# Performance work log

Hardware: AMD Instinct MI355X
Metric: run time of the kernel (lower is better)

## Reference

```python
import jax, jax.numpy as jnp
import numpy as np

NUM_HEADS = 8
ALPHA = 4.0  # spikingjelly sigmoid surrogate default

@jax.custom_vjp
def spike(x):
    return (x >= 0.0).astype(x.dtype)

def _spike_fwd(x):
    return spike(x), x

def _spike_bwd(x, g):
    s = jax.nn.sigmoid(ALPHA * x)
    return (g * ALPHA * s * (1.0 - s),)

spike.defvjp(_spike_fwd, _spike_bwd)

def lif(x, v_th=1.0, tau=2.0):
    # multi-step LIF over leading T dim; v_reset=0, hard reset, detach_reset
    def step(v, xt):
        h = v + (xt - v) / tau
        s = spike(h - v_th)
        v_new = h * (1.0 - jax.lax.stop_gradient(s))
        return v_new, s
    _, out = jax.lax.scan(step, jnp.zeros_like(x[0]), x)
    return out

def bn(x, gamma, beta, mean, var, eps=1e-5):
    # inference BatchNorm2d on (N,C,H,W)
    inv = gamma / jnp.sqrt(var + eps)
    return x * inv[None, :, None, None] + (beta - mean * inv)[None, :, None, None]

def conv1x1(x, w, b=None):
    # x: (N,C,H,W), w: (O,C)
    y = jnp.einsum('nchw,oc->nohw', x, w)
    if b is not None:
        y = y + b[None, :, None, None]
    return y

def setup_inputs() -> dict:
    key = jax.random.key(0)
    ks = jax.random.split(key, 20)
    T, B, C, H, W = 4, 32, 384, 14, 14
    d = {
        'x': jax.random.normal(ks[0], (T, B, C, H, W), jnp.float32),
        'q_w': jax.random.normal(ks[1], (C, C), jnp.float32) * (1.0 / np.sqrt(C)),
        'q_gamma': jax.random.uniform(ks[2], (C,), jnp.float32),
        'q_beta': jax.random.normal(ks[3], (C,), jnp.float32) * 0.1,
        'q_mean': jax.random.normal(ks[4], (C,), jnp.float32) * 0.1,
        'q_var': jax.random.uniform(ks[5], (C,), jnp.float32) + 0.5,
        'k_w': jax.random.normal(ks[6], (C, C), jnp.float32) * (1.0 / np.sqrt(C)),
        'k_gamma': jax.random.uniform(ks[7], (C,), jnp.float32),
        'k_beta': jax.random.normal(ks[8], (C,), jnp.float32) * 0.1,
        'k_mean': jax.random.normal(ks[9], (C,), jnp.float32) * 0.1,
        'k_var': jax.random.uniform(ks[10], (C,), jnp.float32) + 0.5,
        'proj_w': jax.random.normal(ks[11], (C, C), jnp.float32) * (1.0 / np.sqrt(C)),
        'proj_b': jax.random.normal(ks[12], (C,), jnp.float32) * 0.1,
        'proj_gamma': jax.random.uniform(ks[13], (C,), jnp.float32),
        'proj_beta': jax.random.normal(ks[14], (C,), jnp.float32) * 0.1,
        'proj_mean': jax.random.normal(ks[15], (C,), jnp.float32) * 0.1,
        'proj_var': jax.random.uniform(ks[16], (C,), jnp.float32) + 0.5,
    }
    return d

def reference(x, q_w, q_gamma, q_beta, q_mean, q_var,
              k_w, k_gamma, k_beta, k_mean, k_var,
              proj_w, proj_b, proj_gamma, proj_beta, proj_mean, proj_var):
    T, B, C, H, W = x.shape
    dh = C // NUM_HEADS
    xf = x.reshape(T * B, C, H, W)
    # Q branch: conv1x1 -> BN -> multistep LIF
    q = bn(conv1x1(xf, q_w), q_gamma, q_beta, q_mean, q_var).reshape(T, B, C, H, W)
    q = lif(q).reshape(T, B, NUM_HEADS, dh, H, W)
    # K branch
    k = bn(conv1x1(xf, k_w), k_gamma, k_beta, k_mean, k_var).reshape(T, B, C, H, W)
    k = lif(k).reshape(T, B, NUM_HEADS, dh, H, W)
    # sum-pool attention: sum q over head feature dim, spike it, gate k
    qs = jnp.sum(q, axis=3, keepdims=True)          # (T,B,heads,1,H,W)
    attn = lif(qs, v_th=0.5)
    y = (attn * k).reshape(T * B, C, H, W)
    # output projection: conv1x1(+bias) -> BN -> LIF
    y = bn(conv1x1(y, proj_w, proj_b), proj_gamma, proj_beta, proj_mean, proj_var)
    y = lif(y.reshape(T, B, C, H, W))
    return y
```

## Files before the change

### kernel.cpp

```cpp
#include <hip/hip_runtime.h>

#define C_DIM 384
#define S_DIM 196
#define CS_   (C_DIM * S_DIM)
#define BCS   (32 * CS_)
#define NELEM (128 * CS_)
#define NBS   6272

typedef _Float16 half8  __attribute__((ext_vector_type(8)));
typedef float    floatx4 __attribute__((ext_vector_type(4)));

__device__ __forceinline__ void gl_lds16(const _Float16* g, _Float16* l) {
    __builtin_amdgcn_global_load_lds(
        (const __attribute__((address_space(1))) unsigned int*)g,
        (__attribute__((address_space(3))) unsigned int*)l, 16, 0, 0);
}

__global__ __launch_bounds__(256)
void split_w(const float* __restrict__ qw, const float* __restrict__ kw,
             const float* __restrict__ pw,
             const float* qg, const float* qb, const float* qm, const float* qv,
             const float* kg, const float* kb, const float* km, const float* kv,
             _Float16* __restrict__ Wq0, _Float16* __restrict__ Wq1,
             _Float16* __restrict__ Wp0, _Float16* __restrict__ Wp1,
             float2* __restrict__ invsh)
{
    const int i = blockIdx.x * 256 + threadIdx.x;
    const int NQ = 768 * C_DIM;
    if (i < NQ) {
        const int o = i / C_DIM, c = i - o * C_DIM;
        const float v = (o < 384) ? qw[o * C_DIM + c] : kw[(o - 384) * C_DIM + c];
        const _Float16 h0 = (_Float16)v;
        Wq0[i] = h0;
        Wq1[i] = (_Float16)((v - (float)h0) * 4096.0f);
    } else if (i < NQ + C_DIM * C_DIM) {
        const int j = i - NQ;
        const float v = pw[j];
        const _Float16 h0 = (_Float16)v;
        Wp0[j] = h0;
        Wp1[j] = (_Float16)((v - (float)h0) * 4096.0f);
    }
    if (i < 768) {
        float g, b, m, vv;
        if (i < 384) { g = qg[i]; b = qb[i]; m = qm[i]; vv = qv[i]; }
        else         { g = kg[i-384]; b = kb[i-384]; m = km[i-384]; vv = kv[i-384]; }
        const float inv = g / sqrtf(vv + 1e-5f);
        invsh[i] = make_float2(inv, b - m * inv);
    }
}

__global__ __launch_bounds__(256)
void split_x(const float* __restrict__ X,
             _Float16* __restrict__ X0, _Float16* __restrict__ X1)
{
    __shared__ float tile[32][201];
    const int tb = blockIdx.x;
    const int tt = tb >> 5, b = tb & 31;
    const int c0 = blockIdx.y * 32;
    const int t  = threadIdx.x;
    for (int idx = t; idx < 32 * S_DIM; idx += 256) {
        const int cc = idx / S_DIM, s = idx - cc * S_DIM;
        tile[cc][s] = X[(size_t)tb * CS_ + (c0 + cc) * S_DIM + s];
    }
    __syncthreads();
    for (int idx = t; idx < 32 * S_DIM; idx += 256) {
        const int s = idx >> 5, cc = idx & 31;
        const float v = tile[cc][s];
        const _Float16 h0 = (_Float16)v;
        const size_t off = ((size_t)(b * S_DIM + s) * 4 + tt) * C_DIM + c0 + cc;
        X0[off] = h0;
        X1[off] = (_Float16)((v - (float)h0) * 4096.0f);
    }
}

__global__ __launch_bounds__(256, 3)
void qk_mfma(const _Float16* __restrict__ A0, const _Float16* __restrict__ A1,
             const _Float16* __restrict__ B0, const _Float16* __restrict__ B1,
             const float2* __restrict__ invsh,
             unsigned char* __restrict__ spkQ, unsigned char* __restrict__ spkK)
{
    __shared__ __align__(16) _Float16 As0[128 * 32];
    __shared__ __align__(16) _Float16 As1[128 * 32];
    __shared__ __align__(16) _Float16 Bs0[128 * 32];
    __shared__ __align__(16) _Float16 Bs1[128 * 32];

    const int t    = threadIdx.x;
    const int wave = t >> 6, lane = t & 63;
    const int m0 = blockIdx.x * 128;
    const int o0 = blockIdx.y * 128;

    const int wR   = wave * 32;
    const int sRow = lane >> 2;
    const int sCol = (((lane & 3) ^ ((sRow >> 1) & 3))) << 3;

    const int lo = lane & 15, quad = lane >> 4;
    const int oq = (wave >> 1) * 64, mq = (wave & 1) * 64;
    const int rdC = (quad ^ ((lo >> 1) & 3)) << 3;

    floatx4 acc[4][4];
    #pragma unroll
    for (int i = 0; i < 4; ++i)
        #pragma unroll
        for (int j = 0; j < 4; ++j) acc[i][j] = (floatx4)0.0f;

    for (int kt = 0; kt < 12; ++kt) {
        __syncthreads();
        const int kb = kt * 32;
        #pragma unroll
        for (int u = 0; u < 2; ++u) {
            const int R = wR + u * 16;
            const size_t ga = (size_t)(o0 + R + sRow) * C_DIM + kb + sCol;
            const size_t gb = (size_t)(m0 + R + sRow) * C_DIM + kb + sCol;
            gl_lds16(A0 + ga, &As0[R * 32]);
            gl_lds16(A1 + ga, &As1[R * 32]);
            gl_lds16(B0 + gb, &Bs0[R * 32]);
            gl_lds16(B1 + gb, &Bs1[R * 32]);
        }
        __syncthreads();

        half8 a0F[4], a1F[4], b0F[4], b1F[4];
        #pragma unroll
        for (int i = 0; i < 4; ++i) {
            const int ra = (oq + i * 16 + lo) * 32 + rdC;
            a0F[i] = *(const half8*)&As0[ra];
            a1F[i] = *(const half8*)&As1[ra];
        }
        #pragma unroll
        for (int j = 0; j < 4; ++j) {
            const int rb = (mq + j * 16 + lo) * 32 + rdC;
            b0F[j] = *(const half8*)&Bs0[rb];
            b1F[j] = *(const half8*)&Bs1[rb];
        }
        #pragma unroll
        for (int i = 0; i < 4; ++i) {
            const half8 aS = a0F[i] * (_Float16)4096.0f;
            #pragma unroll
            for (int j = 0; j < 4; ++j) {
                acc[i][j] = __builtin_amdgcn_mfma_f32_16x16x32_f16(
                    a0F[i], b1F[j], acc[i][j], 0, 0, 0);
                acc[i][j] = __builtin_amdgcn_mfma_f32_16x16x32_f16(
                    a1F[i], b0F[j], acc[i][j], 0, 0, 0);
                acc[i][j] = __builtin_amdgcn_mfma_f32_16x16x32_f16(
                    aS,     b0F[j], acc[i][j], 0, 0, 0);
            }
        }
    }

    __syncthreads();
    unsigned char* sb = (unsigned char*)As0;
    #pragma unroll
    for (int i = 0; i < 4; ++i) {
        #pragma unroll
        for (int r = 0; r < 4; ++r) {
            const int o = o0 + oq + i * 16 + quad * 4 + r;
            const float2 is = invsh[o];
            const float inv = is.x * (1.0f / 4096.0f);
            const float sh  = is.y;
            #pragma unroll
            for (int j = 0; j < 4; ++j) {
                const float xv = acc[i][j][r] * inv + sh;
                const int g = lane & ~3;
                const float x0 = __shfl(xv, g + 0);
                const float x1 = __shfl(xv, g + 1);
                const float x2 = __shfl(xv, g + 2);
                const float x3 = __shfl(xv, g + 3);
                if ((lane & 3) == 0) {
                    float xs[4] = {x0, x1, x2, x3};
                    float v = 0.0f; int bits = 0;
                    #pragma unroll
                    for (int tt = 0; tt < 4; ++tt) {
                        const float h = v + (xs[tt] - v) * 0.5f;
                        const int sp = (h >= 1.0f);
                        v = sp ? 0.0f : h;
                        bits |= sp << tt;
                    }
                    const int bsl = (mq + j * 16 + lo) >> 2;
                    const int ol  = oq + i * 16 + quad * 4 + r;
                    sb[bsl * 128 + ol] = (unsigned char)bits;
                }
            }
        }
    }
    __syncthreads();
    {
        unsigned char* base = (o0 < 384) ? spkQ : spkK;
        const int o0c = (o0 < 384) ? o0 : o0 - 384;
        const int row = t >> 3, ch = t & 7;
        const uint4 v = *(const uint4*)&sb[row * 128 + ch * 16];
        *(uint4*)(base + (size_t)((m0 >> 2) + row) * C_DIM + o0c + ch * 16) = v;
    }
}

__global__ __launch_bounds__(256)
void attn_compute(const unsigned char* __restrict__ spkQ,
                  unsigned char* __restrict__ attnB)
{
    const int idx = blockIdx.x * 256 + threadIdx.x;
    if (idx >= NBS * 8) return;
    const int bs = idx >> 3, head = idx & 7;
    const unsigned long long* p =
        (const unsigned long long*)(spkQ + (size_t)bs * C_DIM + head * 48);
    int qs[4] = {0, 0, 0, 0};
    #pragma unroll
    for (int u = 0; u < 6; ++u) {
        const unsigned long long v = p[u];
        qs[0] += __popcll(v & 0x0101010101010101ull);
        qs[1] += __popcll(v & 0x0202020202020202ull);
        qs[2] += __popcll(v & 0x0404040404040404ull);
        qs[3] += __popcll(v & 0x0808080808080808ull);
    }
    float va = 0.0f;
    int bits = 0;
    #pragma unroll
    for (int t = 0; t < 4; ++t) {
        const float h = va + ((float)qs[t] - va) * 0.5f;
        const int a = (h >= 0.5f);
        va = a ? 0.0f : h;
        bits |= a << t;
    }
    attnB[idx] = (unsigned char)bits;
}

__global__ __launch_bounds__(256, 3)
void proj_mfma(const _Float16* __restrict__ A0, const _Float16* __restrict__ A1,
               const unsigned char* __restrict__ spkK,
               const unsigned char* __restrict__ attnB,
               const float* __restrict__ bias, const float2* __restrict__ invsh,
               float* __restrict__ out)
{
    __shared__ __align__(16) _Float16 As0[128 * 32];
    __shared__ __align__(16) _Float16 As1[128 * 32];
    __shared__ __align__(16) _Float16 Bs0[128 * 32];

    const int t    = threadIdx.x;
    const int wave = t >> 6, lane = t & 63;
    const int m0 = blockIdx.x * 128;
    const int o0 = blockIdx.y * 128;

    const int wR   = wave * 32;
    const int sRow = lane >> 2;
    const int sCol = (((lane & 3) ^ ((sRow >> 1) & 3))) << 3;
    const int gC8  = (lane & 3) << 3;
    const int pC8  = sCol;

    const int lo = lane & 15, quad = lane >> 4;
    const int oq = (wave >> 1) * 64, mq = (wave & 1) * 64;
    const int rdC = (quad ^ ((lo >> 1) & 3)) << 3;

    const int bsL[2] = { (m0 + wR +  0 + sRow) >> 2, (m0 + wR + 16 + sRow) >> 2 };
    const int ttL    = (m0 + wR + sRow) & 3;

    floatx4 acc[4][4];
    #pragma unroll
    for (int i = 0; i < 4; ++i)
        #pragma unroll
        for (int j = 0; j < 4; ++j) acc[i][j] = (floatx4)0.0f;

    unsigned long long rk[2];
    int rab[2];
    {
        const int head0 = gC8 / 48;
        #pragma unroll
        for (int u = 0; u < 2; ++u) {
            rk[u]  = *(const unsigned long long*)(spkK + (size_t)bsL[u] * C_DIM + gC8);
            rab[u] = (attnB[bsL[u] * 8 + head0] >> ttL) & 1;
        }
    }

    for (int kt = 0; kt < 12; ++kt) {
        __syncthreads();
        const int kb = kt * 32;
        #pragma unroll
        for (int u = 0; u < 2; ++u) {
            const int R = wR + u * 16;
            half8 bv;
            #pragma unroll
            for (int e = 0; e < 8; ++e)
                bv[e] = (_Float16)(float)((int)(rk[u] >> (8 * e + ttL)) & rab[u] & 1);
            *(half8*)&Bs0[(R + sRow) * 32 + pC8] = bv;
            const size_t ga = (size_t)(o0 + R + sRow) * C_DIM + kb + sCol;
            gl_lds16(A0 + ga, &As0[R * 32]);
            gl_lds16(A1 + ga, &As1[R * 32]);
        }
        if (kt < 11) {
            const int kb2  = (kt + 1) * 32;
            const int head = (kb2 + gC8) / 48;
            #pragma unroll
            for (int u = 0; u < 2; ++u) {
                rk[u]  = *(const unsigned long long*)(spkK + (size_t)bsL[u] * C_DIM + kb2 + gC8);
                rab[u] = (attnB[bsL[u] * 8 + head] >> ttL) & 1;
            }
        }
        __syncthreads();

        half8 a0F[4], a1F[4], bF[4];
        #pragma unroll
        for (int i = 0; i < 4; ++i) {
            const int ra = (oq + i * 16 + lo) * 32 + rdC;
            a0F[i] = *(const half8*)&As0[ra];
            a1F[i] = *(const half8*)&As1[ra];
        }
        #pragma unroll
        for (int j = 0; j < 4; ++j)
            bF[j] = *(const half8*)&Bs0[(mq + j * 16 + lo) * 32 + rdC];

        #pragma unroll
        for (int i = 0; i < 4; ++i) {
            const half8 aS = a0F[i] * (_Float16)4096.0f;
            #pragma unroll
            for (int j = 0; j < 4; ++j) {
                acc[i][j] = __builtin_amdgcn_mfma_f32_16x16x32_f16(
                    a1F[i], bF[j], acc[i][j], 0, 0, 0);
                acc[i][j] = __builtin_amdgcn_mfma_f32_16x16x32_f16(
                    aS,     bF[j], acc[i][j], 0, 0, 0);
            }
        }
    }

    #pragma unroll
    for (int i = 0; i < 4; ++i) {
        #pragma unroll
        for (int r = 0; r < 4; ++r) {
            const int o  = o0 + oq + i * 16 + quad * 4 + r;
            const float2 is = invsh[o];
            const float bv = bias[o];
            #pragma unroll
            for (int j = 0; j < 4; ++j) {
                const float p  = acc[i][j][r] * (1.0f / 4096.0f);
                const float zv = (p + bv) * is.x + is.y;
                const int g = lane & ~3;
                const float z0 = __shfl(zv, g + 0);
                const float z1 = __shfl(zv, g + 1);
                const float z2 = __shfl(zv, g + 2);
                const float z3 = __shfl(zv, g + 3);
                if ((lane & 3) == 0) {
                    float zs[4] = {z0, z1, z2, z3};
                    const int bs = (m0 + mq + j * 16 + lo) >> 2;
                    const int b  = bs / S_DIM;
                    const int s  = bs - b * S_DIM;
                    float* op = out + (size_t)b * CS_ + o * S_DIM + s;
                    float v = 0.0f;
                    #pragma unroll
                    for (int tt = 0; tt < 4; ++tt) {
                        const float h = v + (zs[tt] - v) * 0.5f;
                        const int sp = (h >= 1.0f);
                        v = sp ? 0.0f : h;
                        op[(size_t)tt * BCS] = sp ? 1.0f : 0.0f;
                    }
                }
            }
        }
    }
}

extern "C" void kernel_launch(void* const* d_in, const int* in_sizes, int n_in,
                              void* d_out, int out_size, void* d_ws, size_t ws_size,
                              hipStream_t stream)
{
    const float* x          = (const float*)d_in[0];
    const float* q_w        = (const float*)d_in[1];
    const float* q_gamma    = (const float*)d_in[2];
    const float* q_beta     = (const float*)d_in[3];
    const float* q_mean     = (const float*)d_in[4];
    const float* q_var      = (const float*)d_in[5];
    const float* k_w        = (const float*)d_in[6];
    const float* k_gamma    = (const float*)d_in[7];
    const float* k_beta     = (const float*)d_in[8];
    const float* k_mean     = (const float*)d_in[9];
    const float* k_var      = (const float*)d_in[10];
    const float* proj_w     = (const float*)d_in[11];
    const float* proj_b     = (const float*)d_in[12];
    const float* proj_gamma = (const float*)d_in[13];
    const float* proj_beta  = (const float*)d_in[14];
    const float* proj_mean  = (const float*)d_in[15];
    const float* proj_var   = (const float*)d_in[16];
    float* out = (float*)d_out;

    _Float16* h0 = (_Float16*)d_ws;
    _Float16* h1 = h0 + NELEM;
    _Float16* Wq0 = h1 + NELEM;
    _Float16* Wq1 = Wq0 + 768 * C_DIM;
    _Float16* Wp0 = Wq1 + 768 * C_DIM;
    _Float16* Wp1 = Wp0 + C_DIM * C_DIM;
    float2*   invshQ = (float2*)(Wp1 + C_DIM * C_DIM);
    float2*   invshP = invshQ + 768;
    unsigned char* spkQ  = (unsigned char*)(invshP + 384);
    unsigned char* spkK  = spkQ + (size_t)NBS * C_DIM;
    unsigned char* attnB = spkK + (size_t)NBS * C_DIM;

    split_w<<<1728, 256, 0, stream>>>(q_w, k_w, proj_w,
                                      q_gamma, q_beta, q_mean, q_var,
                                      k_gamma, k_beta, k_mean, k_var,
                                      Wq0, Wq1, Wp0, Wp1, invshQ);
    {
        struct L { static __global__ void k(const float* g, const float* b,
                                            const float* m, const float* v,
                                            float2* is) {
            const int i = blockIdx.x * 64 + threadIdx.x;
            if (i < 384) {
                const float inv = g[i] / sqrtf(v[i] + 1e-5f);
                is[i] = make_float2(inv, b[i] - m[i] * inv);
            }
        } };
        L::k<<<6, 64, 0, stream>>>(proj_gamma, proj_beta, proj_mean, proj_var,
                                   invshP);
    }
    split_x<<<dim3(128, 12), 256, 0, stream>>>(x, h0, h1);

    qk_mfma<<<dim3(196, 6), 256, 0, stream>>>(Wq0, Wq1, h0, h1, invshQ,
                                              spkQ, spkK);
    attn_compute<<<196, 256, 0, stream>>>(spkQ, attnB);
    proj_mfma<<<dim3(196, 3), 256, 0, stream>>>(Wp0, Wp1, spkK, attnB,
                                                proj_b, invshP, out);
}
```

Before: 232.2 us.

## Swap MFMA operand roles so each lane holds all four timesteps in-register

The MFMA operands are swapped so the activation (m) dimension sits on the accumulator's 4-row axis. Each lane then holds the four consecutive timesteps of one (bs, channel) in its own acc registers. The LIF epilogues in both GEMM kernels run per lane without the four-way shuffles and lane-0-only branches. The Q/K kernel also drops the LDS staging and its two barriers, writing spike bytes straight to global memory. The trade is scattered byte and float stores that are less coalesced than the previous uint4 store.

```diff
diff --git a/kernel.cpp b/kernel.cpp
--- a/kernel.cpp
+++ b/kernel.cpp
@@ -118,76 +118,56 @@
         }
         __syncthreads();
 
-        half8 a0F[4], a1F[4], b0F[4], b1F[4];
+        half8 w0F[4], w1F[4], x0F[4], x1F[4];
+        #pragma unroll
+        for (int j = 0; j < 4; ++j) {
+            const int ra = (oq + j * 16 + lo) * 32 + rdC;
+            w0F[j] = *(const half8*)&As0[ra];
+            w1F[j] = *(const half8*)&As1[ra];
+        }
         #pragma unroll
         for (int i = 0; i < 4; ++i) {
-            const int ra = (oq + i * 16 + lo) * 32 + rdC;
-            a0F[i] = *(const half8*)&As0[ra];
-            a1F[i] = *(const half8*)&As1[ra];
-        }
-        #pragma unroll
-        for (int j = 0; j < 4; ++j) {
-            const int rb = (mq + j * 16 + lo) * 32 + rdC;
-            b0F[j] = *(const half8*)&Bs0[rb];
-            b1F[j] = *(const half8*)&Bs1[rb];
+            const int rb = (mq + i * 16 + lo) * 32 + rdC;
+            x0F[i] = *(const half8*)&Bs0[rb];
+            x1F[i] = *(const half8*)&Bs1[rb];
         }
         #pragma unroll
         for (int i = 0; i < 4; ++i) {
-            const half8 aS = a0F[i] * (_Float16)4096.0f;
+            const half8 xS = x0F[i] * (_Float16)4096.0f;
             #pragma unroll
             for (int j = 0; j < 4; ++j) {
                 acc[i][j] = __builtin_amdgcn_mfma_f32_16x16x32_f16(
-                    a0F[i], b1F[j], acc[i][j], 0, 0, 0);
-                acc[i][j] = __builtin_amdgcn_mfma_f32_16x16x32_f16(
-                    a1F[i], b0F[j], acc[i][j], 0, 0, 0);
-                acc[i][j] = __builtin_amdgcn_mfma_f32_16x16x32_f16(
-                    aS,     b0F[j], acc[i][j], 0, 0, 0);
-            }
-        }
-    }
-
-    __syncthreads();
-    unsigned char* sb = (unsigned char*)As0;
-    #pragma unroll
-    for (int i = 0; i < 4; ++i) {
-        #pragma unroll
-        for (int r = 0; r < 4; ++r) {
-            const int o = o0 + oq + i * 16 + quad * 4 + r;
-            const float2 is = invsh[o];
-            const float inv = is.x * (1.0f / 4096.0f);
-            const float sh  = is.y;
-            #pragma unroll
-            for (int j = 0; j < 4; ++j) {
+                    x0F[i], w1F[j], acc[i][j], 0, 0, 0);
+                acc[i][j] = __builtin_amdgcn_mfma_f32_16x16x32_f16(
+                    x1F[i], w0F[j], acc[i][j], 0, 0, 0);
+                acc[i][j] = __builtin_amdgcn_mfma_f32_16x16x32_f16(
+                    xS,     w0F[j], acc[i][j], 0, 0, 0);
+            }
+        }
+    }
+
+    #pragma unroll
+    for (int j = 0; j < 4; ++j) {
+        const int o = o0 + oq + j * 16 + lo;
+        const float2 is = invsh[o];
+        const float inv = is.x * (1.0f / 4096.0f);
+        const float sh  = is.y;
+        unsigned char* base = (o < 384) ? spkQ : spkK;
+        const int orow = (o < 384) ? o : o - 384;
+        #pragma unroll
+        for (int i = 0; i < 4; ++i) {
+            const int bs = ((m0 + mq + i * 16) >> 2) + quad;
+            float v = 0.0f; int bits = 0;
+            #pragma unroll
+            for (int r = 0; r < 4; ++r) {
                 const float xv = acc[i][j][r] * inv + sh;
-                const int g = lane & ~3;
-                const float x0 = __shfl(xv, g + 0);
-                const float x1 = __shfl(xv, g + 1);
-                const float x2 = __shfl(xv, g + 2);
-                const float x3 = __shfl(xv, g + 3);
-                if ((lane & 3) == 0) {
-                    float xs[4] = {x0, x1, x2, x3};
-                    float v = 0.0f; int bits = 0;
-                    #pragma unroll
-                    for (int tt = 0; tt < 4; ++tt) {
-                        const float h = v + (xs[tt] - v) * 0.5f;
-                        const int sp = (h >= 1.0f);
-                        v = sp ? 0.0f : h;
-                        bits |= sp << tt;
-                    }
-                    const int bsl = (mq + j * 16 + lo) >> 2;
-                    const int ol  = oq + i * 16 + quad * 4 + r;
-                    sb[bsl * 128 + ol] = (unsigned char)bits;
-                }
-            }
-        }
-    }
-    __syncthreads();
-    {
-        unsigned char* base = (o0 < 384) ? spkQ : spkK;
-        const int o0c = (o0 < 384) ? o0 : o0 - 384;
-        const int row = t >> 3, ch = t & 7;
-        const uint4 v = *(const uint4*)&sb[row * 128 + ch * 16];
-        *(uint4*)(base + (size_t)((m0 >> 2) + row) * C_DIM + o0c + ch * 16) = v;
+                const float h = v + (xv - v) * 0.5f;
+                const int sp = (h >= 1.0f);
+                v = sp ? 0.0f : h;
+                bits |= sp << r;
+            }
+            base[(size_t)bs * C_DIM + orow] = (unsigned char)bits;
+        }
     }
 }
 
@@ -293,61 +273,50 @@
         }
         __syncthreads();
 
-        half8 a0F[4], a1F[4], bF[4];
+        half8 w0F[4], w1F[4], yF[4];
+        #pragma unroll
+        for (int j = 0; j < 4; ++j) {
+            const int ra = (oq + j * 16 + lo) * 32 + rdC;
+            w0F[j] = *(const half8*)&As0[ra];
+            w1F[j] = *(const half8*)&As1[ra];
+        }
+        #pragma unroll
+        for (int i = 0; i < 4; ++i)
+            yF[i] = *(const half8*)&Bs0[(mq + i * 16 + lo) * 32 + rdC];
+
+        #pragma unroll
+        for (int j = 0; j < 4; ++j) {
+            const half8 wS = w0F[j] * (_Float16)4096.0f;
+            #pragma unroll
+            for (int i = 0; i < 4; ++i) {
+                acc[i][j] = __builtin_amdgcn_mfma_f32_16x16x32_f16(
+                    yF[i], w1F[j], acc[i][j], 0, 0, 0);
+                acc[i][j] = __builtin_amdgcn_mfma_f32_16x16x32_f16(
+                    yF[i], wS,     acc[i][j], 0, 0, 0);
+            }
+        }
+    }
+
+    #pragma unroll
+    for (int j = 0; j < 4; ++j) {
+        const int o = o0 + oq + j * 16 + lo;
+        const float2 is = invsh[o];
+        const float bv = bias[o];
         #pragma unroll
         for (int i = 0; i < 4; ++i) {
-            const int ra = (oq + i * 16 + lo) * 32 + rdC;
-            a0F[i] = *(const half8*)&As0[ra];
-            a1F[i] = *(const half8*)&As1[ra];
-        }
-        #pragma unroll
-        for (int j = 0; j < 4; ++j)
-            bF[j] = *(const half8*)&Bs0[(mq + j * 16 + lo) * 32 + rdC];
-
-        #pragma unroll
-        for (int i = 0; i < 4; ++i) {
-            const half8 aS = a0F[i] * (_Float16)4096.0f;
-            #pragma unroll
-            for (int j = 0; j < 4; ++j) {
-                acc[i][j] = __builtin_amdgcn_mfma_f32_16x16x32_f16(
-                    a1F[i], bF[j], acc[i][j], 0, 0, 0);
-                acc[i][j] = __builtin_amdgcn_mfma_f32_16x16x32_f16(
-                    aS,     bF[j], acc[i][j], 0, 0, 0);
-            }
-        }
-    }
-
-    #pragma unroll
-    for (int i = 0; i < 4; ++i) {
-        #pragma unroll
-        for (int r = 0; r < 4; ++r) {
-            const int o  = o0 + oq + i * 16 + quad * 4 + r;
-            const float2 is = invsh[o];
-            const float bv = bias[o];
-            #pragma unroll
-            for (int j = 0; j < 4; ++j) {
-                const float p  = acc[i][j][r] * (1.0f / 4096.0f);
-                const float zv = (p + bv) * is.x + is.y;
-                const int g = lane & ~3;
-                const float z0 = __shfl(zv, g + 0);
-                const float z1 = __shfl(zv, g + 1);
-                const float z2 = __shfl(zv, g + 2);
-                const float z3 = __shfl(zv, g + 3);
-                if ((lane & 3) == 0) {
-                    float zs[4] = {z0, z1, z2, z3};
-                    const int bs = (m0 + mq + j * 16 + lo) >> 2;
-                    const int b  = bs / S_DIM;
-                    const int s  = bs - b * S_DIM;
-                    float* op = out + (size_t)b * CS_ + o * S_DIM + s;
-                    float v = 0.0f;
-                    #pragma unroll
-                    for (int tt = 0; tt < 4; ++tt) {
-                        const float h = v + (zs[tt] - v) * 0.5f;
-                        const int sp = (h >= 1.0f);
-                        v = sp ? 0.0f : h;
-                        op[(size_t)tt * BCS] = sp ? 1.0f : 0.0f;
-                    }
-                }
+            const int bs = ((m0 + mq + i * 16) >> 2) + quad;
+            const int b  = bs / S_DIM;
+            const int s  = bs - b * S_DIM;
+            float* op = out + (size_t)b * CS_ + o * S_DIM + s;
+            float v = 0.0f;
+            #pragma unroll
+            for (int r = 0; r < 4; ++r) {
+                const float p = acc[i][j][r] * (1.0f / 4096.0f);
+                const float z = (p + bv) * is.x + is.y;
+                const float h = v + (z - v) * 0.5f;
+                const int sp = (h >= 1.0f);
+                v = sp ? 0.0f : h;
+                op[(size_t)r * BCS] = sp ? 1.0f : 0.0f;
             }
         }
     }
```

New measurement: 218.6 us. 5.9% less time.
